# Optimization experiments

Measured on AMD Instinct MI355X. Metric: run time of the kernel, lower is better.

The kernel has to match this reference:

```python
import jax, jax.numpy as jnp
import numpy as np

D_IN = 256
D_BIAS = 128
H = 8
DH = 32
B = 2
L = 512
SCALE = 1.0 / np.sqrt(DH)


def _layernorm(x, g, b, eps=1e-5):
    m = jnp.mean(x, axis=-1, keepdims=True)
    v = jnp.var(x, axis=-1, keepdims=True)
    return (x - m) / jnp.sqrt(v + eps) * g + b


def setup_inputs() -> dict:
    key = jax.random.key(0)
    ks = jax.random.split(key, 10)
    w = lambda k, sh, scale: (jax.random.normal(k, sh) * scale).astype(jnp.float32)
    return {
        "x": jax.random.normal(ks[0], (B, L, D_IN), dtype=jnp.float32),
        "bias": jax.random.normal(ks[1], (B, L, L, D_BIAS), dtype=jnp.float32),
        "mask": jax.random.randint(ks[2], (B, L), 0, 2, dtype=jnp.int32),
        "ln_in_g": jnp.ones((D_IN,), jnp.float32),
        "ln_in_b": jnp.zeros((D_IN,), jnp.float32),
        "ln_b_g": jnp.ones((D_BIAS,), jnp.float32),
        "ln_b_b": jnp.zeros((D_BIAS,), jnp.float32),
        "Wq": w(ks[3], (D_IN, H * DH), 0.06),   # xavier-ish scale
        "Wk": w(ks[4], (D_IN, H * DH), 0.06),
        "Wv": w(ks[5], (D_IN, H * DH), 0.06),
        "Wb": w(ks[6], (D_BIAS, H), 0.09),       # lecun normal scale
        "Wg": w(ks[7], (D_IN, H * DH), 0.06),
        "bg": jnp.ones((H * DH,), jnp.float32),  # nn.init.ones_(to_g.bias)
        "Wo": w(ks[8], (H * DH, D_IN), 0.06),
        "bo": jnp.zeros((D_IN,), jnp.float32),
    }


def reference(x, bias, mask, ln_in_g, ln_in_b, ln_b_g, ln_b_b,
              Wq, Wk, Wv, Wb, Wg, bg, Wo, bo):
    Bb, Ll, _ = x.shape
    inv = (mask == 0)                      # True = masked (torch: mask = mask == 0)
    x_safe = jnp.nan_to_num(x)
    b_safe = jnp.nan_to_num(bias)
    xn = _layernorm(x_safe, ln_in_g, ln_in_b)
    bn = _layernorm(b_safe, ln_b_g, ln_b_b)

    q = (xn @ Wq).reshape(Bb, Ll, H, DH)
    k = (xn @ Wk).reshape(Bb, Ll, H, DH) * SCALE
    v = (xn @ Wv).reshape(Bb, Ll, H, DH)
    bias_h = bn @ Wb                       # [B, L, L, H]
    gate = jax.nn.sigmoid(xn @ Wg + bg)    # [B, L, H*DH]

    attn = jnp.einsum('bqhd,bkhd->bqkh', q, k) + bias_h   # [B, q, k, H]
    mask_2d = inv[:, :, None] | inv[:, None, :]            # [B, q, k]
    attn = jnp.where(mask_2d[..., None], -1e9, attn)
    attn = jax.nn.softmax(attn, axis=-2)   # softmax over key dim

    out = jnp.einsum('bqkh,bkhd->bqhd', attn, v).reshape(Bb, Ll, H * DH)
    out = (gate * out) @ Wo + bo
    out = jnp.where(inv[..., None], 0.0, out)
    return out
```

## Files before the change

### kernel.cpp

```cpp
#include <hip/hip_runtime.h>
#include <cstddef>

#define QK_SCALE 0.17677669529663687f

#define FMA4(acc, sc, c) \
    acc.x = fmaf(sc, c.x, acc.x); acc.y = fmaf(sc, c.y, acc.y); \
    acc.z = fmaf(sc, c.z, acc.z); acc.w = fmaf(sc, c.w, acc.w);
#define SCL4(dst, s, v) \
    dst.x = s*v.x; dst.y = s*v.y; dst.z = s*v.z; dst.w = s*v.w;

__device__ __forceinline__ float hred16(float4 dA, float4 dB, int sg) {
    float4 give = (sg & 1) ? dA : dB;
    float4 keep = (sg & 1) ? dB : dA;
    keep.x += __shfl_xor(give.x, 1); keep.y += __shfl_xor(give.y, 1);
    keep.z += __shfl_xor(give.z, 1); keep.w += __shfl_xor(give.w, 1);
    float g0 = (sg & 2) ? keep.x : keep.z;
    float g1 = (sg & 2) ? keep.y : keep.w;
    float e0 = (sg & 2) ? keep.z : keep.x;
    float e1 = (sg & 2) ? keep.w : keep.y;
    e0 += __shfl_xor(g0, 2); e1 += __shfl_xor(g1, 2);
    float g2 = (sg & 4) ? e0 : e1;
    float d  = (sg & 4) ? e1 : e0;
    d += __shfl_xor(g2, 4);
    d += __shfl_xor(d, 8);
    return d;
}

__global__ __launch_bounds__(256) void kA(
    const float* __restrict__ x, const int* __restrict__ mask,
    const float* __restrict__ lng, const float* __restrict__ lnb,
    const float* __restrict__ Wq, const float* __restrict__ Wk,
    const float* __restrict__ Wv, const float* __restrict__ Wg,
    const float* __restrict__ bgv,
    const float* __restrict__ lnbg, const float* __restrict__ lnbb,
    const float* __restrict__ Wb, const float* __restrict__ bias,
    const float* __restrict__ bo,
    float* __restrict__ qg, float* __restrict__ ktg,
    float* __restrict__ vg, float* __restrict__ gateg,
    float* __restrict__ bh, float* __restrict__ out)
{
    __shared__ float xn_s[4][256];
    __shared__ int kl_s[512];
    __shared__ int cnt_s[8];
    const int tid = threadIdx.x;
    const int w = tid >> 6, lane = tid & 63;

    if (blockIdx.x >= 256) {
        const int bid2 = blockIdx.x - 256;
        const int b    = bid2 >> 10;
        const int q    = (bid2 >> 1) & 511;
        const int half = bid2 & 1;
        if (mask[(b << 9) + q] == 0) return;

        int mreg[2]; unsigned long long bal[2];
        #pragma unroll
        for (int c = 0; c < 2; ++c) {
            mreg[c] = (mask[(b << 9) + c*256 + tid] != 0);
            bal[c] = __ballot(mreg[c]);
            if (lane == 0) cnt_s[(c << 2) + w] = __popcll(bal[c]);
        }
        __syncthreads();
        int nk = 0;
        #pragma unroll
        for (int j = 0; j < 8; ++j) nk += cnt_s[j];
        #pragma unroll
        for (int c = 0; c < 2; ++c) {
            int idx = (c << 2) + w, base = 0;
            #pragma unroll
            for (int j = 0; j < 8; ++j) base += (j < idx) ? cnt_s[j] : 0;
            if (mreg[c])
                kl_s[base + __popcll(bal[c] & ((1ull << lane) - 1ull))] = c*256 + tid;
        }

        const int rq = lane >> 4;
        const int sg = lane & 15;
        const int h  = ((sg & 1) << 2) + (sg & 2) + ((sg >> 2) & 1);
        float4 cA0[4], cB0[4], cA1[4], cB1[4];
        float4 s1a = {0,0,0,0}, s1b = {0,0,0,0}, s2a = {0,0,0,0}, s2b = {0,0,0,0};
        #pragma unroll
        for (int j = 0; j < 4; ++j) {
            int c0 = 4*sg + j, c1 = 64 + 4*sg + j;
            float4 wa = *reinterpret_cast<const float4*>(Wb + c0*8);
            float4 wb = *reinterpret_cast<const float4*>(Wb + c0*8 + 4);
            float ga = lnbg[c0], bbv = lnbb[c0];
            SCL4(cA0[j], ga, wa); SCL4(cB0[j], ga, wb);
            FMA4(s1a, ga, wa); FMA4(s1b, ga, wb);
            FMA4(s2a, bbv, wa); FMA4(s2b, bbv, wb);
            float4 wa1 = *reinterpret_cast<const float4*>(Wb + c1*8);
            float4 wb1 = *reinterpret_cast<const float4*>(Wb + c1*8 + 4);
            float ga1 = lnbg[c1], bbv1 = lnbb[c1];
            SCL4(cA1[j], ga1, wa1); SCL4(cB1[j], ga1, wb1);
            FMA4(s1a, ga1, wa1); FMA4(s1b, ga1, wb1);
            FMA4(s2a, bbv1, wa1); FMA4(s2b, bbv1, wb1);
        }
        const float S1 = hred16(s1a, s1b, sg);
        const float S2 = hred16(s2a, s2b, sg);

        const float4* brow = reinterpret_cast<const float4*>(
            bias + (size_t)((b << 9) + q) * 512 * 128);
        __syncthreads();

        for (int p = 0; (p << 5) + half < nk; ++p) {
            const int i = (((p << 4) + (w << 2) + rq) << 1) + half;
            if (i < nk) {
                const int k = kl_s[i];
                const float4* bp = brow + (size_t)k * 32;
                float4 v0 = bp[sg];
                float4 v1 = bp[16 + sg];

                float s  = v0.x+v0.y+v0.z+v0.w + v1.x+v1.y+v1.z+v1.w;
                float ss = v0.x*v0.x; ss = fmaf(v0.y,v0.y, ss); ss = fmaf(v0.z,v0.z, ss);
                ss = fmaf(v0.w,v0.w, ss); ss = fmaf(v1.x,v1.x, ss); ss = fmaf(v1.y,v1.y, ss);
                ss = fmaf(v1.z,v1.z, ss); ss = fmaf(v1.w,v1.w, ss);

                float4 dA = {0.f,0.f,0.f,0.f}, dB = {0.f,0.f,0.f,0.f};
                FMA4(dA, v0.x, cA0[0]); FMA4(dB, v0.x, cB0[0]);
                FMA4(dA, v0.y, cA0[1]); FMA4(dB, v0.y, cB0[1]);
                FMA4(dA, v0.z, cA0[2]); FMA4(dB, v0.z, cB0[2]);
                FMA4(dA, v0.w, cA0[3]); FMA4(dB, v0.w, cB0[3]);
                FMA4(dA, v1.x, cA1[0]); FMA4(dB, v1.x, cB1[0]);
                FMA4(dA, v1.y, cA1[1]); FMA4(dB, v1.y, cB1[1]);
                FMA4(dA, v1.z, cA1[2]); FMA4(dB, v1.z, cB1[2]);
                FMA4(dA, v1.w, cA1[3]); FMA4(dB, v1.w, cB1[3]);

                float dsum = hred16(dA, dB, sg);
                #pragma unroll
                for (int m = 1; m < 16; m <<= 1) {
                    s  += __shfl_xor(s,  m);
                    ss += __shfl_xor(ss, m);
                }
                float mean = s * (1.f/128.f);
                float rstd = rsqrtf(ss*(1.f/128.f) - mean*mean + 1e-5f);
                if (sg < 8)
                    bh[((size_t)((b*8 + h) * 512) + q) * 512 + k] = rstd * (dsum - mean*S1) + S2;
            }
        }
        return;
    }

    const int gr0 = blockIdx.x * 4;
    const int row = gr0 + w;

    float4 xv = *reinterpret_cast<const float4*>(x + (size_t)row * 256 + lane * 4);
    float s  = xv.x + xv.y + xv.z + xv.w;
    float ss = xv.x*xv.x + xv.y*xv.y + xv.z*xv.z + xv.w*xv.w;
    #pragma unroll
    for (int m = 1; m < 64; m <<= 1) { s += __shfl_xor(s, m); ss += __shfl_xor(ss, m); }
    float mean = s * (1.f/256.f);
    float rstd = rsqrtf(ss*(1.f/256.f) - mean*mean + 1e-5f);
    float4 g4 = *reinterpret_cast<const float4*>(lng + lane*4);
    float4 b4 = *reinterpret_cast<const float4*>(lnb + lane*4);
    float4 xn;
    xn.x = (xv.x-mean)*rstd*g4.x + b4.x;
    xn.y = (xv.y-mean)*rstd*g4.y + b4.y;
    xn.z = (xv.z-mean)*rstd*g4.z + b4.z;
    xn.w = (xv.w-mean)*rstd*g4.w + b4.w;
    *reinterpret_cast<float4*>(&xn_s[w][lane*4]) = xn;

    float bov = bo[tid];
    #pragma unroll
    for (int r = 0; r < 4; ++r) {
        int gr = gr0 + r;
        out[(size_t)gr * 256 + tid] = (mask[gr] == 0) ? 0.f : bov;
    }
    __syncthreads();

    const float* W = (w == 0) ? Wq : (w == 1) ? Wk : (w == 2) ? Wv : Wg;
    const int col = lane << 2;
    float a[4][4];
    #pragma unroll
    for (int r = 0; r < 4; ++r)
        #pragma unroll
        for (int c = 0; c < 4; ++c) a[r][c] = 0.f;

    #pragma unroll 4
    for (int c = 0; c < 256; c += 4) {
        float4 w0 = *reinterpret_cast<const float4*>(W + (size_t)(c+0)*256 + col);
        float4 w1 = *reinterpret_cast<const float4*>(W + (size_t)(c+1)*256 + col);
        float4 w2 = *reinterpret_cast<const float4*>(W + (size_t)(c+2)*256 + col);
        float4 w3 = *reinterpret_cast<const float4*>(W + (size_t)(c+3)*256 + col);
        #pragma unroll
        for (int r = 0; r < 4; ++r) {
            float4 xr = *reinterpret_cast<const float4*>(&xn_s[r][c]);
            a[r][0] = fmaf(xr.x,w0.x, fmaf(xr.y,w1.x, fmaf(xr.z,w2.x, fmaf(xr.w,w3.x, a[r][0]))));
            a[r][1] = fmaf(xr.x,w0.y, fmaf(xr.y,w1.y, fmaf(xr.z,w2.y, fmaf(xr.w,w3.y, a[r][1]))));
            a[r][2] = fmaf(xr.x,w0.z, fmaf(xr.y,w1.z, fmaf(xr.z,w2.z, fmaf(xr.w,w3.z, a[r][2]))));
            a[r][3] = fmaf(xr.x,w0.w, fmaf(xr.y,w1.w, fmaf(xr.z,w2.w, fmaf(xr.w,w3.w, a[r][3]))));
        }
    }

    if (w == 0) {
        #pragma unroll
        for (int r = 0; r < 4; ++r) {
            float4 o; o.x=a[r][0]; o.y=a[r][1]; o.z=a[r][2]; o.w=a[r][3];
            *reinterpret_cast<float4*>(qg + (size_t)(gr0+r)*256 + col) = o;
        }
    } else if (w == 1) {
        #pragma unroll
        for (int r = 0; r < 4; ++r) {
            int gr = gr0 + r, gb = gr >> 9, gl = gr & 511;
            #pragma unroll
            for (int jj = 0; jj < 4; ++jj) {
                int c2 = col + jj;
                ktg[((size_t)(gb*8 + (c2>>5))*32 + (c2&31))*512 + gl] = a[r][jj] * QK_SCALE;
            }
        }
    } else if (w == 2) {
        #pragma unroll
        for (int r = 0; r < 4; ++r) {
            float4 o; o.x=a[r][0]; o.y=a[r][1]; o.z=a[r][2]; o.w=a[r][3];
            *reinterpret_cast<float4*>(vg + (size_t)(gr0+r)*256 + col) = o;
        }
    } else {
        float4 bg4 = *reinterpret_cast<const float4*>(bgv + col);
        #pragma unroll
        for (int r = 0; r < 4; ++r) {
            float4 o;
            o.x = 1.f/(1.f + __expf(-(a[r][0] + bg4.x)));
            o.y = 1.f/(1.f + __expf(-(a[r][1] + bg4.y)));
            o.z = 1.f/(1.f + __expf(-(a[r][2] + bg4.z)));
            o.w = 1.f/(1.f + __expf(-(a[r][3] + bg4.w)));
            *reinterpret_cast<float4*>(gateg + (size_t)(gr0+r)*256 + col) = o;
        }
    }
}

__global__ __launch_bounds__(512, 2) void kB(
    const float* __restrict__ qg, const float* __restrict__ ktg,
    const float* __restrict__ vg, const float* __restrict__ gateg,
    const float* __restrict__ bh, const int* __restrict__ mask,
    const float* __restrict__ Wo, float* __restrict__ out)
{
    __shared__ float kv_s[8192];
    __shared__ float q_s[32][32];
    __shared__ float p_s[8][4][128];
    __shared__ float att_s[32][32];

    const int tid = threadIdx.x;
    const int bid = blockIdx.x;
    const int b  = bid >> 7;
    const int h  = (bid >> 4) & 7;
    const int qt = bid & 15;
    const int w = tid >> 6, lane = tid & 63;
    const int ql = lane >> 5, dd2 = lane & 31;
    const int mq = b << 9;
    const int q0 = qt << 5;
    const int qw = q0 + (w << 2);

    {
        int qr = tid >> 4, dd = (tid & 15) << 1;
        float2 v = *reinterpret_cast<const float2*>(
            qg + (size_t)(mq + q0 + qr) * 256 + (h << 5) + dd);
        *reinterpret_cast<float2*>(&q_s[qr][dd]) = v;
    }

    float mrun[4] = {-1e30f, -1e30f, -1e30f, -1e30f};
    float sden[4] = {0.f, 0.f, 0.f, 0.f};
    float a0A=0.f, a0B=0.f, a1A=0.f, a1B=0.f;

    for (int kt2 = 0; kt2 < 4; ++kt2) {
        const int k0 = kt2 << 7;
        __syncthreads();
        {
            int d = tid >> 4, kk = (tid & 15) << 3;
            const float* src = ktg + ((size_t)((b << 3) + h) * 32 + d) * 512 + k0 + kk;
            float4 a4 = *reinterpret_cast<const float4*>(src);
            float4 b4 = *reinterpret_cast<const float4*>(src + 4);
            *reinterpret_cast<float4*>(&kv_s[d * 128 + kk])     = a4;
            *reinterpret_cast<float4*>(&kv_s[d * 128 + kk + 4]) = b4;
            int k = tid >> 2, dd = (tid & 3) << 3;
            const float* vs = vg + (size_t)(mq + k0 + k) * 256 + (h << 5) + dd;
            float4 c4 = *reinterpret_cast<const float4*>(vs);
            float4 e4 = *reinterpret_cast<const float4*>(vs + 4);
            *reinterpret_cast<float4*>(&kv_s[4096 + k * 32 + dd])     = c4;
            *reinterpret_cast<float4*>(&kv_s[4096 + k * 32 + dd + 4]) = e4;
        }
        __syncthreads();

        const int mkA = (mask[mq + k0 + lane] == 0);
        const int mkB = (mask[mq + k0 + 64 + lane] == 0);

        float bhA[4], bhB[4];
        #pragma unroll
        for (int qq = 0; qq < 4; ++qq) {
            const float* r = bh + (((size_t)(b*8 + h) * 512) + qw + qq) * 512 + k0;
            bhA[qq] = r[lane];
            bhB[qq] = r[64 + lane];
        }

        float lA[4] = {0.f,0.f,0.f,0.f}, lB[4] = {0.f,0.f,0.f,0.f};
        #pragma unroll
        for (int d4 = 0; d4 < 32; d4 += 4) {
            float4 q4[4];
            #pragma unroll
            for (int qq = 0; qq < 4; ++qq)
                q4[qq] = *reinterpret_cast<const float4*>(&q_s[(w << 2) + qq][d4]);
            float kv0[4], kv1[4];
            #pragma unroll
            for (int j = 0; j < 4; ++j) {
                kv0[j] = kv_s[(d4 + j) * 128 + lane];
                kv1[j] = kv_s[(d4 + j) * 128 + 64 + lane];
            }
            #pragma unroll
            for (int qq = 0; qq < 4; ++qq) {
                lA[qq] = fmaf(q4[qq].x, kv0[0], lA[qq]);
                lA[qq] = fmaf(q4[qq].y, kv0[1], lA[qq]);
                lA[qq] = fmaf(q4[qq].z, kv0[2], lA[qq]);
                lA[qq] = fmaf(q4[qq].w, kv0[3], lA[qq]);
                lB[qq] = fmaf(q4[qq].x, kv1[0], lB[qq]);
                lB[qq] = fmaf(q4[qq].y, kv1[1], lB[qq]);
                lB[qq] = fmaf(q4[qq].z, kv1[2], lB[qq]);
                lB[qq] = fmaf(q4[qq].w, kv1[3], lB[qq]);
            }
        }

        float corr4[4];
        #pragma unroll
        for (int qq = 0; qq < 4; ++qq) {
            float la = mkA ? -1e30f : (lA[qq] + bhA[qq]);
            float lb = mkB ? -1e30f : (lB[qq] + bhB[qq]);
            float mx = fmaxf(la, lb);
            #pragma unroll
            for (int m = 1; m < 64; m <<= 1) mx = fmaxf(mx, __shfl_xor(mx, m));
            float mnew = fmaxf(mrun[qq], mx);
            float corr = __expf(mrun[qq] - mnew);
            float pa = mkA ? 0.f : __expf(la - mnew);
            float pb = mkB ? 0.f : __expf(lb - mnew);
            float ts = pa + pb;
            #pragma unroll
            for (int m = 1; m < 64; m <<= 1) ts += __shfl_xor(ts, m);
            sden[qq] = sden[qq] * corr + ts;
            mrun[qq] = mnew;
            corr4[qq] = corr;
            p_s[w][qq][lane]      = pa;
            p_s[w][qq][64 + lane] = pb;
        }

        float c0 = ql ? corr4[1] : corr4[0];
        float c1 = ql ? corr4[3] : corr4[2];
        a0A *= c0; a0B *= c0; a1A *= c1; a1B *= c1;
        const float* pr0 = p_s[w][ql];
        const float* pr1 = p_s[w][ql + 2];
        #pragma unroll 4
        for (int k = 0; k < 128; k += 8) {
            float4 p0a = *reinterpret_cast<const float4*>(pr0 + k);
            float4 p0b = *reinterpret_cast<const float4*>(pr0 + k + 4);
            float4 p1a = *reinterpret_cast<const float4*>(pr1 + k);
            float4 p1b = *reinterpret_cast<const float4*>(pr1 + k + 4);
            float v0 = kv_s[4096 + (k+0)*32 + dd2], v1 = kv_s[4096 + (k+1)*32 + dd2];
            float v2 = kv_s[4096 + (k+2)*32 + dd2], v3 = kv_s[4096 + (k+3)*32 + dd2];
            float v4 = kv_s[4096 + (k+4)*32 + dd2], v5 = kv_s[4096 + (k+5)*32 + dd2];
            float v6 = kv_s[4096 + (k+6)*32 + dd2], v7 = kv_s[4096 + (k+7)*32 + dd2];
            a0A = fmaf(p0a.x,v0, fmaf(p0a.y,v1, fmaf(p0a.z,v2, fmaf(p0a.w,v3, a0A))));
            a0B = fmaf(p0b.x,v4, fmaf(p0b.y,v5, fmaf(p0b.z,v6, fmaf(p0b.w,v7, a0B))));
            a1A = fmaf(p1a.x,v0, fmaf(p1a.y,v1, fmaf(p1a.z,v2, fmaf(p1a.w,v3, a1A))));
            a1B = fmaf(p1b.x,v4, fmaf(p1b.y,v5, fmaf(p1b.z,v6, fmaf(p1b.w,v7, a1B))));
        }
    }

    {
        float sd0 = ql ? sden[1] : sden[0];
        float sd1 = ql ? sden[3] : sden[2];
        float g0 = gateg[(size_t)(mq + qw + ql) * 256 + (h << 5) + dd2];
        float g1 = gateg[(size_t)(mq + qw + ql + 2) * 256 + (h << 5) + dd2];
        int iv0 = (mask[mq + qw + ql] == 0);
        int iv1 = (mask[mq + qw + ql + 2] == 0);
        att_s[(w << 2) + ql][dd2]     = iv0 ? 0.f : (a0A + a0B) / sd0 * g0;
        att_s[(w << 2) + ql + 2][dd2] = iv1 ? 0.f : (a1A + a1B) / sd1 * g1;
    }
    __syncthreads();

    {
        const float* wsrc = Wo + (size_t)h * 32 * 256;
        for (int i = tid; i < 2048; i += 512)
            *reinterpret_cast<float4*>(&kv_s[i << 2]) =
                *reinterpret_cast<const float4*>(wsrc + (i << 2));
    }
    __syncthreads();

    {
        const int c2 = tid & 255, qh = tid >> 8;
        float acc[16];
        #pragma unroll
        for (int i = 0; i < 16; ++i) acc[i] = 0.f;
        #pragma unroll
        for (int d4 = 0; d4 < 32; d4 += 4) {
            float w0 = kv_s[(d4+0)*256 + c2];
            float w1 = kv_s[(d4+1)*256 + c2];
            float w2 = kv_s[(d4+2)*256 + c2];
            float w3 = kv_s[(d4+3)*256 + c2];
            #pragma unroll
            for (int i = 0; i < 16; ++i) {
                float4 a4 = *reinterpret_cast<const float4*>(&att_s[(qh << 4) + i][d4]);
                acc[i] = fmaf(a4.x,w0, fmaf(a4.y,w1, fmaf(a4.z,w2, fmaf(a4.w,w3, acc[i]))));
            }
        }
        #pragma unroll
        for (int i = 0; i < 16; ++i)
            atomicAdd(out + (size_t)(mq + q0 + (qh << 4) + i) * 256 + c2, acc[i]);
    }
}

extern "C" void kernel_launch(void* const* d_in, const int* in_sizes, int n_in,
                              void* d_out, int out_size, void* d_ws, size_t ws_size,
                              hipStream_t stream)
{
    const float* x    = (const float*)d_in[0];
    const float* bias = (const float*)d_in[1];
    const int*   mask = (const int*)d_in[2];
    const float* lng  = (const float*)d_in[3];
    const float* lnb  = (const float*)d_in[4];
    const float* lnbg = (const float*)d_in[5];
    const float* lnbb = (const float*)d_in[6];
    const float* Wq   = (const float*)d_in[7];
    const float* Wk   = (const float*)d_in[8];
    const float* Wv   = (const float*)d_in[9];
    const float* Wb   = (const float*)d_in[10];
    const float* Wg   = (const float*)d_in[11];
    const float* bgv  = (const float*)d_in[12];
    const float* Wo   = (const float*)d_in[13];
    const float* bo   = (const float*)d_in[14];
    float* out = (float*)d_out;

    float* ws    = (float*)d_ws;
    float* qg    = ws;
    float* ktg   = qg    + 262144;
    float* vg    = ktg   + 262144;
    float* gateg = vg    + 262144;
    float* bhg   = gateg + 262144;

    hipLaunchKernelGGL(kA, dim3(2304), dim3(256), 0, stream,
        x, mask, lng, lnb, Wq, Wk, Wv, Wg, bgv, lnbg, lnbb, Wb, bias, bo,
        qg, ktg, vg, gateg, bhg, out);
    hipLaunchKernelGGL(kB, dim3(256), dim3(512), 0, stream,
        qg, ktg, vg, gateg, bhg, mask, Wo, out);
}
```

Measured before the change: 75.99 us.

## Rebalance work split: one bias block per query row, halve attention query tile

The bias-projection part of kA now processes a whole query row per block instead of splitting the keys across two blocks, cutting that grid from 2048 to 1024 blocks and halving the per-block Wb/LN coefficient setup. kB drops its query tile from 32 to 16 rows, so it launches 512 blocks, each wave handles 2 query rows and each thread holds one output accumulator. This raises kB parallelism on a GPU with many CUs but reloads K/V tiles and Wo twice as often and doubles the atomic adds to the output.

```diff
diff --git a/kernel.cpp b/kernel.cpp
--- a/kernel.cpp
+++ b/kernel.cpp
@@ -47,9 +47,8 @@
 
     if (blockIdx.x >= 256) {
         const int bid2 = blockIdx.x - 256;
-        const int b    = bid2 >> 10;
-        const int q    = (bid2 >> 1) & 511;
-        const int half = bid2 & 1;
+        const int b = bid2 >> 9;
+        const int q = bid2 & 511;
         if (mask[(b << 9) + q] == 0) return;
 
         int mreg[2]; unsigned long long bal[2];
@@ -100,8 +99,8 @@
             bias + (size_t)((b << 9) + q) * 512 * 128);
         __syncthreads();
 
-        for (int p = 0; (p << 5) + half < nk; ++p) {
-            const int i = (((p << 4) + (w << 2) + rq) << 1) + half;
+        for (int p = 0; (p << 4) < nk; ++p) {
+            const int i = (p << 4) + (w << 2) + rq;
             if (i < nk) {
                 const int k = kl_s[i];
                 const float4* bp = brow + (size_t)k * 32;
@@ -232,31 +231,29 @@
     const float* __restrict__ Wo, float* __restrict__ out)
 {
     __shared__ float kv_s[8192];
-    __shared__ float q_s[32][32];
-    __shared__ float p_s[8][4][128];
-    __shared__ float att_s[32][32];
+    __shared__ float q_s[16][32];
+    __shared__ float p_s[8][2][128];
+    __shared__ float att_s[16][32];
 
     const int tid = threadIdx.x;
     const int bid = blockIdx.x;
-    const int b  = bid >> 7;
-    const int h  = (bid >> 4) & 7;
-    const int qt = bid & 15;
+    const int b  = bid >> 8;
+    const int h  = (bid >> 5) & 7;
+    const int qt = bid & 31;
     const int w = tid >> 6, lane = tid & 63;
     const int ql = lane >> 5, dd2 = lane & 31;
     const int mq = b << 9;
-    const int q0 = qt << 5;
-    const int qw = q0 + (w << 2);
+    const int q0 = qt << 4;
+    const int qw = q0 + (w << 1);
 
     {
-        int qr = tid >> 4, dd = (tid & 15) << 1;
-        float2 v = *reinterpret_cast<const float2*>(
-            qg + (size_t)(mq + q0 + qr) * 256 + (h << 5) + dd);
-        *reinterpret_cast<float2*>(&q_s[qr][dd]) = v;
-    }
-
-    float mrun[4] = {-1e30f, -1e30f, -1e30f, -1e30f};
-    float sden[4] = {0.f, 0.f, 0.f, 0.f};
-    float a0A=0.f, a0B=0.f, a1A=0.f, a1B=0.f;
+        int qr = tid >> 5, dd = tid & 31;
+        q_s[qr][dd] = qg[(size_t)(mq + q0 + qr) * 256 + (h << 5) + dd];
+    }
+
+    float mrun[2] = {-1e30f, -1e30f};
+    float sden[2] = {0.f, 0.f};
+    float aA = 0.f, aB = 0.f;
 
     for (int kt2 = 0; kt2 < 4; ++kt2) {
         const int k0 = kt2 << 7;
@@ -280,21 +277,20 @@
         const int mkA = (mask[mq + k0 + lane] == 0);
         const int mkB = (mask[mq + k0 + 64 + lane] == 0);
 
-        float bhA[4], bhB[4];
-        #pragma unroll
-        for (int qq = 0; qq < 4; ++qq) {
+        float bhA[2], bhB[2];
+        #pragma unroll
+        for (int qq = 0; qq < 2; ++qq) {
             const float* r = bh + (((size_t)(b*8 + h) * 512) + qw + qq) * 512 + k0;
             bhA[qq] = r[lane];
             bhB[qq] = r[64 + lane];
         }
 
-        float lA[4] = {0.f,0.f,0.f,0.f}, lB[4] = {0.f,0.f,0.f,0.f};
+        float lA[2] = {0.f, 0.f}, lB[2] = {0.f, 0.f};
         #pragma unroll
         for (int d4 = 0; d4 < 32; d4 += 4) {
-            float4 q4[4];
-            #pragma unroll
-            for (int qq = 0; qq < 4; ++qq)
-                q4[qq] = *reinterpret_cast<const float4*>(&q_s[(w << 2) + qq][d4]);
+            float4 q4[2];
+            q4[0] = *reinterpret_cast<const float4*>(&q_s[(w << 1)][d4]);
+            q4[1] = *reinterpret_cast<const float4*>(&q_s[(w << 1) + 1][d4]);
             float kv0[4], kv1[4];
             #pragma unroll
             for (int j = 0; j < 4; ++j) {
@@ -302,7 +298,7 @@
                 kv1[j] = kv_s[(d4 + j) * 128 + 64 + lane];
             }
             #pragma unroll
-            for (int qq = 0; qq < 4; ++qq) {
+            for (int qq = 0; qq < 2; ++qq) {
                 lA[qq] = fmaf(q4[qq].x, kv0[0], lA[qq]);
                 lA[qq] = fmaf(q4[qq].y, kv0[1], lA[qq]);
                 lA[qq] = fmaf(q4[qq].z, kv0[2], lA[qq]);
@@ -314,9 +310,9 @@
             }
         }
 
-        float corr4[4];
-        #pragma unroll
-        for (int qq = 0; qq < 4; ++qq) {
+        float corr2[2];
+        #pragma unroll
+        for (int qq = 0; qq < 2; ++qq) {
             float la = mkA ? -1e30f : (lA[qq] + bhA[qq]);
             float lb = mkB ? -1e30f : (lB[qq] + bhB[qq]);
             float mx = fmaxf(la, lb);
@@ -331,42 +327,32 @@
             for (int m = 1; m < 64; m <<= 1) ts += __shfl_xor(ts, m);
             sden[qq] = sden[qq] * corr + ts;
             mrun[qq] = mnew;
-            corr4[qq] = corr;
+            corr2[qq] = corr;
             p_s[w][qq][lane]      = pa;
             p_s[w][qq][64 + lane] = pb;
         }
 
-        float c0 = ql ? corr4[1] : corr4[0];
-        float c1 = ql ? corr4[3] : corr4[2];
-        a0A *= c0; a0B *= c0; a1A *= c1; a1B *= c1;
-        const float* pr0 = p_s[w][ql];
-        const float* pr1 = p_s[w][ql + 2];
+        float c = ql ? corr2[1] : corr2[0];
+        aA *= c; aB *= c;
+        const float* pr = p_s[w][ql];
         #pragma unroll 4
         for (int k = 0; k < 128; k += 8) {
-            float4 p0a = *reinterpret_cast<const float4*>(pr0 + k);
-            float4 p0b = *reinterpret_cast<const float4*>(pr0 + k + 4);
-            float4 p1a = *reinterpret_cast<const float4*>(pr1 + k);
-            float4 p1b = *reinterpret_cast<const float4*>(pr1 + k + 4);
+            float4 pa4 = *reinterpret_cast<const float4*>(pr + k);
+            float4 pb4 = *reinterpret_cast<const float4*>(pr + k + 4);
             float v0 = kv_s[4096 + (k+0)*32 + dd2], v1 = kv_s[4096 + (k+1)*32 + dd2];
             float v2 = kv_s[4096 + (k+2)*32 + dd2], v3 = kv_s[4096 + (k+3)*32 + dd2];
             float v4 = kv_s[4096 + (k+4)*32 + dd2], v5 = kv_s[4096 + (k+5)*32 + dd2];
             float v6 = kv_s[4096 + (k+6)*32 + dd2], v7 = kv_s[4096 + (k+7)*32 + dd2];
-            a0A = fmaf(p0a.x,v0, fmaf(p0a.y,v1, fmaf(p0a.z,v2, fmaf(p0a.w,v3, a0A))));
-            a0B = fmaf(p0b.x,v4, fmaf(p0b.y,v5, fmaf(p0b.z,v6, fmaf(p0b.w,v7, a0B))));
-            a1A = fmaf(p1a.x,v0, fmaf(p1a.y,v1, fmaf(p1a.z,v2, fmaf(p1a.w,v3, a1A))));
-            a1B = fmaf(p1b.x,v4, fmaf(p1b.y,v5, fmaf(p1b.z,v6, fmaf(p1b.w,v7, a1B))));
+            aA = fmaf(pa4.x,v0, fmaf(pa4.y,v1, fmaf(pa4.z,v2, fmaf(pa4.w,v3, aA))));
+            aB = fmaf(pb4.x,v4, fmaf(pb4.y,v5, fmaf(pb4.z,v6, fmaf(pb4.w,v7, aB))));
         }
     }
 
     {
-        float sd0 = ql ? sden[1] : sden[0];
-        float sd1 = ql ? sden[3] : sden[2];
-        float g0 = gateg[(size_t)(mq + qw + ql) * 256 + (h << 5) + dd2];
-        float g1 = gateg[(size_t)(mq + qw + ql + 2) * 256 + (h << 5) + dd2];
-        int iv0 = (mask[mq + qw + ql] == 0);
-        int iv1 = (mask[mq + qw + ql + 2] == 0);
-        att_s[(w << 2) + ql][dd2]     = iv0 ? 0.f : (a0A + a0B) / sd0 * g0;
-        att_s[(w << 2) + ql + 2][dd2] = iv1 ? 0.f : (a1A + a1B) / sd1 * g1;
+        float sd = ql ? sden[1] : sden[0];
+        float g = gateg[(size_t)(mq + qw + ql) * 256 + (h << 5) + dd2];
+        int iv = (mask[mq + qw + ql] == 0);
+        att_s[(w << 1) + ql][dd2] = iv ? 0.f : (aA + aB) / sd * g;
     }
     __syncthreads();
 
@@ -380,9 +366,9 @@
 
     {
         const int c2 = tid & 255, qh = tid >> 8;
-        float acc[16];
-        #pragma unroll
-        for (int i = 0; i < 16; ++i) acc[i] = 0.f;
+        float acc[8];
+        #pragma unroll
+        for (int i = 0; i < 8; ++i) acc[i] = 0.f;
         #pragma unroll
         for (int d4 = 0; d4 < 32; d4 += 4) {
             float w0 = kv_s[(d4+0)*256 + c2];
@@ -390,14 +376,14 @@
             float w2 = kv_s[(d4+2)*256 + c2];
             float w3 = kv_s[(d4+3)*256 + c2];
             #pragma unroll
-            for (int i = 0; i < 16; ++i) {
-                float4 a4 = *reinterpret_cast<const float4*>(&att_s[(qh << 4) + i][d4]);
+            for (int i = 0; i < 8; ++i) {
+                float4 a4 = *reinterpret_cast<const float4*>(&att_s[(qh << 3) + i][d4]);
                 acc[i] = fmaf(a4.x,w0, fmaf(a4.y,w1, fmaf(a4.z,w2, fmaf(a4.w,w3, acc[i]))));
             }
         }
         #pragma unroll
-        for (int i = 0; i < 16; ++i)
-            atomicAdd(out + (size_t)(mq + q0 + (qh << 4) + i) * 256 + c2, acc[i]);
+        for (int i = 0; i < 8; ++i)
+            atomicAdd(out + (size_t)(mq + q0 + (qh << 3) + i) * 256 + c2, acc[i]);
     }
 }
 
@@ -429,9 +415,9 @@
     float* gateg = vg    + 262144;
     float* bhg   = gateg + 262144;
 
-    hipLaunchKernelGGL(kA, dim3(2304), dim3(256), 0, stream,
+    hipLaunchKernelGGL(kA, dim3(1280), dim3(256), 0, stream,
         x, mask, lng, lnb, Wq, Wk, Wv, Wg, bgv, lnbg, lnbb, Wb, bias, bo,
         qg, ktg, vg, gateg, bhg, out);
-    hipLaunchKernelGGL(kB, dim3(256), dim3(512), 0, stream,
+    hipLaunchKernelGGL(kB, dim3(512), dim3(512), 0, stream,
         qg, ktg, vg, gateg, bhg, mask, Wo, out);
 }
```

New measurement: 77.30 us. No clear change (+1.7%).

## Stage full K/V per head in LDS and merge bias-row halves into one block

Applied to the files above, without the earlier changes.

The attention kernel now loads the entire K and V slices for its batch/head into shared memory once, before the key loop. This removes the per-tile reload and the two barriers per iteration, and the K/V indexing is updated to match. The bias-projection part of the first kernel now uses one block per query row instead of two blocks each taking alternating keys, which shrinks the grid. In exchange, the 128KB LDS buffer limits the attention kernel to one block per CU, loads are no longer overlapped with compute, and the bias phase has fewer, longer blocks.

```diff
diff --git a/kernel.cpp b/kernel.cpp
--- a/kernel.cpp
+++ b/kernel.cpp
@@ -47,9 +47,8 @@
 
     if (blockIdx.x >= 256) {
         const int bid2 = blockIdx.x - 256;
-        const int b    = bid2 >> 10;
-        const int q    = (bid2 >> 1) & 511;
-        const int half = bid2 & 1;
+        const int b = bid2 >> 9;
+        const int q = bid2 & 511;
         if (mask[(b << 9) + q] == 0) return;
 
         int mreg[2]; unsigned long long bal[2];
@@ -100,8 +99,8 @@
             bias + (size_t)((b << 9) + q) * 512 * 128);
         __syncthreads();
 
-        for (int p = 0; (p << 5) + half < nk; ++p) {
-            const int i = (((p << 4) + (w << 2) + rq) << 1) + half;
+        for (int p = 0; (p << 4) < nk; ++p) {
+            const int i = (p << 4) + (w << 2) + rq;
             if (i < nk) {
                 const int k = kl_s[i];
                 const float4* bp = brow + (size_t)k * 32;
@@ -231,7 +230,7 @@
     const float* __restrict__ bh, const int* __restrict__ mask,
     const float* __restrict__ Wo, float* __restrict__ out)
 {
-    __shared__ float kv_s[8192];
+    __shared__ float kv_s[32768];
     __shared__ float q_s[32][32];
     __shared__ float p_s[8][4][128];
     __shared__ float att_s[32][32];
@@ -253,6 +252,23 @@
             qg + (size_t)(mq + q0 + qr) * 256 + (h << 5) + dd);
         *reinterpret_cast<float2*>(&q_s[qr][dd]) = v;
     }
+    {
+        const float* ksrc = ktg + (size_t)((b << 3) + h) * 16384;
+        #pragma unroll
+        for (int j = 0; j < 8; ++j) {
+            int f4 = tid + j * 512;
+            *reinterpret_cast<float4*>(&kv_s[f4 << 2]) =
+                *reinterpret_cast<const float4*>(ksrc + (f4 << 2));
+        }
+        #pragma unroll
+        for (int j = 0; j < 8; ++j) {
+            int f4 = tid + j * 512;
+            int k = f4 >> 3, dd4 = (f4 & 7) << 2;
+            *reinterpret_cast<float4*>(&kv_s[16384 + (f4 << 2)]) =
+                *reinterpret_cast<const float4*>(vg + (size_t)(mq + k) * 256 + (h << 5) + dd4);
+        }
+    }
+    __syncthreads();
 
     float mrun[4] = {-1e30f, -1e30f, -1e30f, -1e30f};
     float sden[4] = {0.f, 0.f, 0.f, 0.f};
@@ -260,23 +276,6 @@
 
     for (int kt2 = 0; kt2 < 4; ++kt2) {
         const int k0 = kt2 << 7;
-        __syncthreads();
-        {
-            int d = tid >> 4, kk = (tid & 15) << 3;
-            const float* src = ktg + ((size_t)((b << 3) + h) * 32 + d) * 512 + k0 + kk;
-            float4 a4 = *reinterpret_cast<const float4*>(src);
-            float4 b4 = *reinterpret_cast<const float4*>(src + 4);
-            *reinterpret_cast<float4*>(&kv_s[d * 128 + kk])     = a4;
-            *reinterpret_cast<float4*>(&kv_s[d * 128 + kk + 4]) = b4;
-            int k = tid >> 2, dd = (tid & 3) << 3;
-            const float* vs = vg + (size_t)(mq + k0 + k) * 256 + (h << 5) + dd;
-            float4 c4 = *reinterpret_cast<const float4*>(vs);
-            float4 e4 = *reinterpret_cast<const float4*>(vs + 4);
-            *reinterpret_cast<float4*>(&kv_s[4096 + k * 32 + dd])     = c4;
-            *reinterpret_cast<float4*>(&kv_s[4096 + k * 32 + dd + 4]) = e4;
-        }
-        __syncthreads();
-
         const int mkA = (mask[mq + k0 + lane] == 0);
         const int mkB = (mask[mq + k0 + 64 + lane] == 0);
 
@@ -298,8 +297,8 @@
             float kv0[4], kv1[4];
             #pragma unroll
             for (int j = 0; j < 4; ++j) {
-                kv0[j] = kv_s[(d4 + j) * 128 + lane];
-                kv1[j] = kv_s[(d4 + j) * 128 + 64 + lane];
+                kv0[j] = kv_s[(d4 + j) * 512 + k0 + lane];
+                kv1[j] = kv_s[(d4 + j) * 512 + k0 + 64 + lane];
             }
             #pragma unroll
             for (int qq = 0; qq < 4; ++qq) {
@@ -341,16 +340,17 @@
         a0A *= c0; a0B *= c0; a1A *= c1; a1B *= c1;
         const float* pr0 = p_s[w][ql];
         const float* pr1 = p_s[w][ql + 2];
+        const int vb = 16384 + k0 * 32 + dd2;
         #pragma unroll 4
         for (int k = 0; k < 128; k += 8) {
             float4 p0a = *reinterpret_cast<const float4*>(pr0 + k);
             float4 p0b = *reinterpret_cast<const float4*>(pr0 + k + 4);
             float4 p1a = *reinterpret_cast<const float4*>(pr1 + k);
             float4 p1b = *reinterpret_cast<const float4*>(pr1 + k + 4);
-            float v0 = kv_s[4096 + (k+0)*32 + dd2], v1 = kv_s[4096 + (k+1)*32 + dd2];
-            float v2 = kv_s[4096 + (k+2)*32 + dd2], v3 = kv_s[4096 + (k+3)*32 + dd2];
-            float v4 = kv_s[4096 + (k+4)*32 + dd2], v5 = kv_s[4096 + (k+5)*32 + dd2];
-            float v6 = kv_s[4096 + (k+6)*32 + dd2], v7 = kv_s[4096 + (k+7)*32 + dd2];
+            float v0 = kv_s[vb + (k+0)*32], v1 = kv_s[vb + (k+1)*32];
+            float v2 = kv_s[vb + (k+2)*32], v3 = kv_s[vb + (k+3)*32];
+            float v4 = kv_s[vb + (k+4)*32], v5 = kv_s[vb + (k+5)*32];
+            float v6 = kv_s[vb + (k+6)*32], v7 = kv_s[vb + (k+7)*32];
             a0A = fmaf(p0a.x,v0, fmaf(p0a.y,v1, fmaf(p0a.z,v2, fmaf(p0a.w,v3, a0A))));
             a0B = fmaf(p0b.x,v4, fmaf(p0b.y,v5, fmaf(p0b.z,v6, fmaf(p0b.w,v7, a0B))));
             a1A = fmaf(p1a.x,v0, fmaf(p1a.y,v1, fmaf(p1a.z,v2, fmaf(p1a.w,v3, a1A))));
@@ -429,7 +429,7 @@
     float* gateg = vg    + 262144;
     float* bhg   = gateg + 262144;
 
-    hipLaunchKernelGGL(kA, dim3(2304), dim3(256), 0, stream,
+    hipLaunchKernelGGL(kA, dim3(1280), dim3(256), 0, stream,
         x, mask, lng, lnb, Wq, Wk, Wv, Wg, bgv, lnbg, lnbb, Wb, bias, bo,
         qg, ktg, vg, gateg, bhg, out);
     hipLaunchKernelGGL(kB, dim3(256), dim3(512), 0, stream,
```

Measured after the change: 78.01 us. 2.7% more time.

## Split bias rows into quarters per block and software-prefetch next key's bias

Applied to the files above, without the earlier changes.

The bias-projection part of kernel A now splits each query row across four blocks instead of two, doubling the grid for that phase. Inside the loop, the next key's bias vectors are loaded into registers before the current key is reduced, a software pipeline that hides global-memory latency. The cost is more register pressure and extra per-block setup: mask ballot and Wb coefficient precompute are repeated in twice as many blocks.

```diff
diff --git a/kernel.cpp b/kernel.cpp
--- a/kernel.cpp
+++ b/kernel.cpp
@@ -47,9 +47,9 @@
 
     if (blockIdx.x >= 256) {
         const int bid2 = blockIdx.x - 256;
-        const int b    = bid2 >> 10;
-        const int q    = (bid2 >> 1) & 511;
-        const int half = bid2 & 1;
+        const int b       = bid2 >> 11;
+        const int q       = (bid2 >> 2) & 511;
+        const int quarter = bid2 & 3;
         if (mask[(b << 9) + q] == 0) return;
 
         int mreg[2]; unsigned long long bal[2];
@@ -100,14 +100,30 @@
             bias + (size_t)((b << 9) + q) * 512 * 128);
         __syncthreads();
 
-        for (int p = 0; (p << 5) + half < nk; ++p) {
-            const int i = (((p << 4) + (w << 2) + rq) << 1) + half;
-            if (i < nk) {
-                const int k = kl_s[i];
-                const float4* bp = brow + (size_t)k * 32;
-                float4 v0 = bp[sg];
-                float4 v1 = bp[16 + sg];
-
+        const int slot = (w << 2) + rq;
+        const int npass = (nk > quarter) ? ((nk - quarter + 63) >> 6) : 0;
+
+        int i_cur = (slot << 2) + quarter;
+        bool v_cur = i_cur < nk;
+        int k_cur = 0; float4 a_cur = {0,0,0,0}, b_cur = {0,0,0,0};
+        if (v_cur) {
+            k_cur = kl_s[i_cur];
+            const float4* bp = brow + (size_t)k_cur * 32;
+            a_cur = bp[sg]; b_cur = bp[16 + sg];
+        }
+
+        for (int p = 0; p < npass; ++p) {
+            const int i_nxt = i_cur + 64;
+            const bool v_nxt = (p + 1 < npass) && (i_nxt < nk);
+            int k_nxt = 0; float4 a_nxt = {0,0,0,0}, b_nxt = {0,0,0,0};
+            if (v_nxt) {
+                k_nxt = kl_s[i_nxt];
+                const float4* bp = brow + (size_t)k_nxt * 32;
+                a_nxt = bp[sg]; b_nxt = bp[16 + sg];
+            }
+
+            if (v_cur) {
+                float4 v0 = a_cur, v1 = b_cur;
                 float s  = v0.x+v0.y+v0.z+v0.w + v1.x+v1.y+v1.z+v1.w;
                 float ss = v0.x*v0.x; ss = fmaf(v0.y,v0.y, ss); ss = fmaf(v0.z,v0.z, ss);
                 ss = fmaf(v0.w,v0.w, ss); ss = fmaf(v1.x,v1.x, ss); ss = fmaf(v1.y,v1.y, ss);
@@ -132,8 +148,11 @@
                 float mean = s * (1.f/128.f);
                 float rstd = rsqrtf(ss*(1.f/128.f) - mean*mean + 1e-5f);
                 if (sg < 8)
-                    bh[((size_t)((b*8 + h) * 512) + q) * 512 + k] = rstd * (dsum - mean*S1) + S2;
-            }
+                    bh[((size_t)((b*8 + h) * 512) + q) * 512 + k_cur] = rstd * (dsum - mean*S1) + S2;
+            }
+
+            i_cur = i_nxt; v_cur = v_nxt; k_cur = k_nxt;
+            a_cur = a_nxt; b_cur = b_nxt;
         }
         return;
     }
@@ -429,7 +448,7 @@
     float* gateg = vg    + 262144;
     float* bhg   = gateg + 262144;
 
-    hipLaunchKernelGGL(kA, dim3(2304), dim3(256), 0, stream,
+    hipLaunchKernelGGL(kA, dim3(4352), dim3(256), 0, stream,
         x, mask, lng, lnb, Wq, Wk, Wv, Wg, bgv, lnbg, lnbb, Wb, bias, bo,
         qg, ktg, vg, gateg, bhg, out);
     hipLaunchKernelGGL(kB, dim3(256), dim3(512), 0, stream,
```

Result: slower. 83.42 us (+9.8%).
